# Performance work log

Hardware: AMD Instinct MI355X
Metric: run time of the kernel (lower is better)

## Reference

```python
import jax, jax.numpy as jnp
import numpy as np

D_MODEL = 1024
D_FFN = 4096
H = 16
D_HEAD = D_MODEL // H
B, L = 2, 2048
EPS = 1e-6


def layer_norm(x, a, b):
    # Matches torch: std is unbiased (ddof=1), and divides by (std + eps)
    mean = jnp.mean(x, axis=-1, keepdims=True)
    var = jnp.sum((x - mean) ** 2, axis=-1, keepdims=True) / (x.shape[-1] - 1)
    std = jnp.sqrt(var)
    return (x - mean) / (std + EPS) * a + b


def setup_inputs() -> dict:
    key = jax.random.key(0)
    ks = jax.random.split(key, 10)
    s = 0.02
    x = jax.random.normal(ks[0], (B, L, D_MODEL), dtype=jnp.float32)
    mask = jnp.tril(jnp.ones((L, L), dtype=jnp.int32))[None, None]  # causal [1,1,L,L]
    return {
        "x": x,
        "mask": mask,
        "Wqkv": jax.random.normal(ks[1], (D_MODEL, 3 * D_MODEL), jnp.float32) * s,
        "bqkv": jnp.zeros((3 * D_MODEL,), jnp.float32),
        "Wo": jax.random.normal(ks[2], (D_MODEL, D_MODEL), jnp.float32) * s,
        "bo": jnp.zeros((D_MODEL,), jnp.float32),
        "W1": jax.random.normal(ks[3], (D_MODEL, D_FFN), jnp.float32) * s,
        "b1": jnp.zeros((D_FFN,), jnp.float32),
        "W2": jax.random.normal(ks[4], (D_FFN, D_MODEL), jnp.float32) * s,
        "b2": jnp.zeros((D_MODEL,), jnp.float32),
        "ln1_a": jnp.ones((D_MODEL,), jnp.float32),
        "ln1_b": jnp.zeros((D_MODEL,), jnp.float32),
        "ln2_a": jnp.ones((D_MODEL,), jnp.float32),
        "ln2_b": jnp.zeros((D_MODEL,), jnp.float32),
    }


def reference(x, mask, Wqkv, bqkv, Wo, bo, W1, b1, W2, b2, ln1_a, ln1_b, ln2_a, ln2_b):
    b, l, d = x.shape
    # --- attention sublayer ---
    qkv = x @ Wqkv + bqkv                                   # [b, l, 3*d]
    qkv = qkv.reshape(b, l, 3, H, D_HEAD)                   # '(three h d)' ordering
    q, k, v = qkv[:, :, 0], qkv[:, :, 1], qkv[:, :, 2]      # each [b, l, h, dh]
    scores = jnp.einsum('bqhd,bkhd->bhqk', q, k) / jnp.sqrt(
        jnp.asarray(D_HEAD, x.dtype))                        # [b, h, lq, lk]
    scores = jnp.where(mask == 0, -jnp.inf, scores)
    p = jax.nn.softmax(scores, axis=-1)
    attn = jnp.einsum('bhqk,bkhd->bqhd', p, v).reshape(b, l, d)
    attn_out = attn @ Wo + bo
    x = layer_norm(x + attn_out, ln1_a, ln1_b)
    # --- MLP sublayer ---
    h = jax.nn.relu(x @ W1 + b1)
    mlp_out = h @ W2 + b2
    return layer_norm(x + mlp_out, ln2_a, ln2_b)
```

## Files before the change

kernel.cpp:

```cpp
#include <hip/hip_runtime.h>

#define D_MODEL 1024
#define D_FFN   4096
#define NH      16
#define DH      64
#define BB      2
#define LL      2048
#define MROWS   (BB * LL)

typedef unsigned short u16;
typedef unsigned int   u32;
typedef short bf16x8 __attribute__((ext_vector_type(8)));
typedef float f32x4  __attribute__((ext_vector_type(4)));

__device__ __forceinline__ float bf2f(u16 u) {
    union { u32 i; float f; } v;
    v.i = ((u32)u) << 16;
    return v.f;
}
__device__ __forceinline__ u16 f2bf(float f) {
    union { float f; u32 i; } v;
    v.f = f;
    u32 x = v.i;
    x += 0x7fffu + ((x >> 16) & 1u);
    return (u16)(x >> 16);
}
__device__ __forceinline__ u32 pack_bf_trunc(float a, float b) {
    return __builtin_amdgcn_perm(__float_as_uint(b), __float_as_uint(a),
                                 0x07060302u);
}

typedef const __attribute__((address_space(1))) u32 gu32;
typedef __attribute__((address_space(3))) u32 lu32;
__device__ __forceinline__ void gload_lds16(const void* g, void* l) {
    __builtin_amdgcn_global_load_lds((gu32*)g, (lu32*)l, 16, 0, 0);
}

__global__ __launch_bounds__(256) void prep_kernel(
    const float* __restrict__ x,    u16* __restrict__ xb,
    const float* __restrict__ Wqkv, u16* __restrict__ Wqkvt,
    const float* __restrict__ Wo,   u16* __restrict__ Wot,
    const float* __restrict__ W1,   u16* __restrict__ W1t,
    const float* __restrict__ W2,   u16* __restrict__ W2t)
{
    __shared__ float tile[64][65];
    const int tid = threadIdx.x;
    const int bi  = blockIdx.x;

    if (bi < 2048) {
        int i = bi * 2048 + tid * 8;
        float4 a = *(const float4*)(x + i);
        float4 b = *(const float4*)(x + i + 4);
        u16 o[8] = {f2bf(a.x), f2bf(a.y), f2bf(a.z), f2bf(a.w),
                    f2bf(b.x), f2bf(b.y), f2bf(b.z), f2bf(b.w)};
        *(uint4*)(xb + i) = *(const uint4*)o;
        return;
    }

    const float* W; u16* Wt; int K, N, t;
    if (bi < 2816)      { W = Wqkv; Wt = Wqkvt; K = 1024; N = 3072; t = bi - 2048; }
    else if (bi < 3072) { W = Wo;   Wt = Wot;   K = 1024; N = 1024; t = bi - 2816; }
    else if (bi < 4096) { W = W1;   Wt = W1t;   K = 1024; N = 4096; t = bi - 3072; }
    else                { W = W2;   Wt = W2t;   K = 4096; N = 1024; t = bi - 4096; }
    const int ntiles = N >> 6;
    const int n0 = (t % ntiles) * 64;
    const int k0 = (t / ntiles) * 64;

    int kr = tid >> 4;
    int nc = (tid & 15) * 4;
    #pragma unroll
    for (int p = 0; p < 4; ++p) {
        float4 v = *(const float4*)&W[(size_t)(k0 + kr + p * 16) * N + n0 + nc];
        tile[kr + p * 16][nc + 0] = v.x;
        tile[kr + p * 16][nc + 1] = v.y;
        tile[kr + p * 16][nc + 2] = v.z;
        tile[kr + p * 16][nc + 3] = v.w;
    }
    __syncthreads();

    int nr = tid >> 2;
    int kc = (tid & 3) * 16;
    u16 o[16];
    #pragma unroll
    for (int j = 0; j < 16; ++j) o[j] = f2bf(tile[kc + j][nr]);
    u16* dst = &Wt[(size_t)(n0 + nr) * K + k0 + kc];
    *(uint4*)dst       = *(const uint4*)&o[0];
    *(uint4*)(dst + 8) = *(const uint4*)&o[8];
}

template <int EPI, int RF32, int OF32, int KS>
__global__ __launch_bounds__(256) void gemm_bt_kernel(
    const u16* __restrict__ A, const u16* __restrict__ Bt,
    const float* __restrict__ bias, const void* __restrict__ resv,
    void* __restrict__ out0v, u16* __restrict__ out1, u16* __restrict__ out2,
    int M, int N, int K)
{
    __shared__ u16 sA[128 * 64];
    __shared__ u16 sB[128 * 64];

    const int tid  = threadIdx.x;
    const int lane = tid & 63;
    const int wave = tid >> 6;
    const int wm   = (wave & 1) * 64;
    const int wn   = (wave >> 1) * 64;
    const int quad = lane >> 4;
    const int l16  = lane & 15;

    const int nb  = gridDim.x;
    const int mb  = gridDim.y;
    const int f   = blockIdx.y * nb + blockIdx.x;
    const int xcd = f & 7;
    const int idx = f >> 3;
    const int rn  = nb >> 1;
    const int rm  = mb >> 2;
    const int n0  = ((xcd & 1) * rn + (idx % rn)) * 128;
    const int ym  = (xcd >> 1) * rm + (idx / rn);

    int s, m0;
    if (KS > 1) {
        const int mt = mb / KS;
        s  = ym / mt;
        m0 = (ym % mt) * 128;
    } else {
        s  = 0;
        m0 = ym * 128;
    }
    const int Kseg = K / KS;
    const int kbeg = s * Kseg;

    f32x4 acc[4][4];
    #pragma unroll
    for (int i = 0; i < 4; ++i)
        #pragma unroll
        for (int j = 0; j < 4; ++j)
            acc[i][j] = (f32x4){0.f, 0.f, 0.f, 0.f};

    const u16* Ablk = A  + (size_t)m0 * K;
    const u16* Bblk = Bt + (size_t)n0 * K;

    for (int k0 = kbeg; k0 < kbeg + Kseg; k0 += 64) {
        #pragma unroll
        for (int i = 0; i < 4; ++i) {
            int chunk = (i * 4 + wave) * 64 + lane;
            int r = chunk >> 3;
            int c = (chunk & 7) ^ (r & 7);
            size_t goff = (size_t)r * K + k0 + c * 8;
            gload_lds16(Ablk + goff, &sA[(i * 4 + wave) * 512]);
            gload_lds16(Bblk + goff, &sB[(i * 4 + wave) * 512]);
        }
        __syncthreads();

        #pragma unroll
        for (int ks = 0; ks < 2; ++ks) {
            bf16x8 af[4], bfr[4];
            #pragma unroll
            for (int i = 0; i < 4; ++i) {
                int R = wm + i * 16 + l16;
                int slot = R * 8 + ((ks * 4 + quad) ^ (R & 7));
                af[i] = *(const bf16x8*)&sA[slot * 8];
            }
            #pragma unroll
            for (int j = 0; j < 4; ++j) {
                int R = wn + j * 16 + l16;
                int slot = R * 8 + ((ks * 4 + quad) ^ (R & 7));
                bfr[j] = *(const bf16x8*)&sB[slot * 8];
            }
            #pragma unroll
            for (int i = 0; i < 4; ++i)
                #pragma unroll
                for (int j = 0; j < 4; ++j)
                    acc[i][j] = __builtin_amdgcn_mfma_f32_16x16x32_bf16(
                        af[i], bfr[j], acc[i][j], 0, 0, 0);
        }
        __syncthreads();
    }

    #pragma unroll
    for (int i = 0; i < 4; ++i) {
        int rowb = m0 + wm + i * 16 + quad * 4;
        #pragma unroll
        for (int j = 0; j < 4; ++j) {
            int col = n0 + wn + j * 16 + l16;
            float bv = (EPI == 3) ? 0.f : bias[col];
            #pragma unroll
            for (int r = 0; r < 4; ++r) {
                int rr = rowb + r;
                float v = acc[i][j][r] + bv;
                if (EPI == 0) {
                    int which = col >> 10;
                    int h     = (col >> 6) & 15;
                    int d     = col & 63;
                    int b     = rr >> 11;
                    int l     = rr & 2047;
                    size_t idx2 = ((size_t)(b * NH + h) * LL + l) * DH + d;
                    u16* o0 = (u16*)out0v;
                    if (which == 0)      o0[idx2]   = f2bf(v * 0.125f);
                    else if (which == 1) out1[idx2] = f2bf(v);
                    else                 out2[idx2] = f2bf(v);
                } else if (EPI == 3) {
                    ((u16*)out0v)[((size_t)s * M + rr) * N + col] = f2bf(v);
                } else {
                    size_t idx2 = (size_t)rr * N + col;
                    if (EPI == 1) {
                        v += RF32 ? ((const float*)resv)[idx2]
                                  : bf2f(((const u16*)resv)[idx2]);
                    } else {
                        v = v > 0.f ? v : 0.f;
                    }
                    if (OF32) ((float*)out0v)[idx2] = v;
                    else      ((u16*)out0v)[idx2]   = f2bf(v);
                }
            }
        }
    }
}

template <int KS, int RF32, int OF32>
__global__ __launch_bounds__(256) void lnfuse_kernel(
    const u16* __restrict__ P, const float* __restrict__ bias,
    const void* __restrict__ resv,
    const float* __restrict__ ga, const float* __restrict__ gb,
    void* __restrict__ outv)
{
    __shared__ float red[8];
    const int tid  = threadIdx.x;
    const int lane = tid & 63;
    const int wave = tid >> 6;
    const size_t row = blockIdx.x;
    const size_t SL  = (size_t)MROWS * D_MODEL;
    const int c = tid * 4;

    float v0, v1, v2, v3;
    {
        float4 bv = *(const float4*)(bias + c);
        v0 = bv.x; v1 = bv.y; v2 = bv.z; v3 = bv.w;
    }
    #pragma unroll
    for (int s = 0; s < KS; ++s) {
        uint2 p = *(const uint2*)(P + s * SL + row * D_MODEL + c);
        v0 += bf2f((u16)p.x); v1 += bf2f((u16)(p.x >> 16));
        v2 += bf2f((u16)p.y); v3 += bf2f((u16)(p.y >> 16));
    }
    if (RF32) {
        float4 r = *(const float4*)((const float*)resv + row * D_MODEL + c);
        v0 += r.x; v1 += r.y; v2 += r.z; v3 += r.w;
    } else {
        uint2 r = *(const uint2*)((const u16*)resv + row * D_MODEL + c);
        v0 += bf2f((u16)r.x); v1 += bf2f((u16)(r.x >> 16));
        v2 += bf2f((u16)r.y); v3 += bf2f((u16)(r.y >> 16));
    }

    float s_ = v0 + v1 + v2 + v3;
    #pragma unroll
    for (int o = 32; o > 0; o >>= 1) s_ += __shfl_xor(s_, o, 64);
    if (lane == 0) red[wave] = s_;
    __syncthreads();
    float mean = (red[0] + red[1] + red[2] + red[3]) * (1.f / 1024.f);

    float d0 = v0 - mean, d1 = v1 - mean, d2 = v2 - mean, d3 = v3 - mean;
    float q = d0 * d0 + d1 * d1 + d2 * d2 + d3 * d3;
    #pragma unroll
    for (int o = 32; o > 0; o >>= 1) q += __shfl_xor(q, o, 64);
    if (lane == 0) red[4 + wave] = q;
    __syncthreads();
    float var = (red[4] + red[5] + red[6] + red[7]) * (1.f / 1023.f);
    float inv = 1.f / (sqrtf(var) + 1e-6f);

    float y0 = d0 * inv * ga[c + 0] + gb[c + 0];
    float y1 = d1 * inv * ga[c + 1] + gb[c + 1];
    float y2 = d2 * inv * ga[c + 2] + gb[c + 2];
    float y3 = d3 * inv * ga[c + 3] + gb[c + 3];
    if (OF32) {
        float4 y = {y0, y1, y2, y3};
        *(float4*)((float*)outv + row * D_MODEL + c) = y;
    } else {
        ushort4 y = {f2bf(y0), f2bf(y1), f2bf(y2), f2bf(y3)};
        *(ushort4*)((u16*)outv + row * D_MODEL + c) = y;
    }
}

__global__ __launch_bounds__(256) void attn_kernel(
    const u16* __restrict__ Q, const u16* __restrict__ K,
    const u16* __restrict__ V, u16* __restrict__ out)
{
    __shared__ u16 ks[64 * 72];
    __shared__ u16 vs[64 * 72];
    __shared__ u16 ps[4][2][16 * 72];

    const int tid  = threadIdx.x;
    const int lane = tid & 63;
    const int wave = tid >> 6;
    const int l16  = lane & 15;
    const int quad = lane >> 4;

    const int f   = blockIdx.x;
    const int xcd = f & 7;
    const int idx = f >> 3;
    const int bh  = xcd * 4 + (idx >> 4);
    const int pr  = idx & 15;
    const int b   = bh >> 4, h = bh & 15;
    const size_t head_off = (size_t)bh * LL * DH;

    const u16* Qh = Q + head_off;
    const u16* Kh = K + head_off;
    const u16* Vh = V + head_off;

    const int qtA = 31 - pr, qtB = pr;
    const int baseA = qtA * 64 + wave * 16;
    const int baseB = qtB * 64 + wave * 16;
    const int qgA   = baseA + l16;
    const int qgB   = baseB + l16;

    const bf16x8 qfA0 = *(const bf16x8*)&Qh[(size_t)qgA * DH + quad * 8];
    const bf16x8 qfA1 = *(const bf16x8*)&Qh[(size_t)qgA * DH + 32 + quad * 8];
    const bf16x8 qfB0 = *(const bf16x8*)&Qh[(size_t)qgB * DH + quad * 8];
    const bf16x8 qfB1 = *(const bf16x8*)&Qh[(size_t)qgB * DH + 32 + quad * 8];

    float lA = 0.f, lB = 0.f;
    f32x4 oA[4], oB[4];
    #pragma unroll
    for (int t = 0; t < 4; ++t) {
        oA[t] = (f32x4){0.f, 0.f, 0.f, 0.f};
        oB[t] = (f32x4){0.f, 0.f, 0.f, 0.f};
    }

    u16* psA = &ps[wave][0][0];
    u16* psB = &ps[wave][1][0];

    const int key = tid >> 2;
    const int kd0 = (tid & 3) * 16;
    const int kp  = tid >> 3;
    const int vd0 = (tid & 7) * 8;

    uint4 kr0, kr1, vr0, vr1;
    {
        const u16* ksrc = Kh + (size_t)key * DH + kd0;
        kr0 = *(const uint4*)ksrc;
        kr1 = *(const uint4*)(ksrc + 8);
        const u16* vsrc = Vh + (size_t)(2 * kp) * DH + vd0;
        vr0 = *(const uint4*)vsrc;
        vr1 = *(const uint4*)(vsrc + DH);
    }

    for (int c = 0; c <= qtA; ++c) {
        const bool doB = (c <= qtB);
        __syncthreads();
        *(uint4*)&ks[key * 72 + kd0]     = kr0;
        *(uint4*)&ks[key * 72 + kd0 + 8] = kr1;
        {
            const u32* w0 = (const u32*)&vr0;
            const u32* w1 = (const u32*)&vr1;
            #pragma unroll
            for (int e = 0; e < 8; ++e) {
                int d = vd0 + e;
                u32 lo = (w0[e >> 1] >> ((e & 1) * 16)) & 0xffffu;
                u32 hi = (w1[e >> 1] >> ((e & 1) * 16)) & 0xffffu;
                int csw = kp ^ (4 * ((d >> 3) & 7));
                *(u32*)&vs[d * 72 + 2 * csw] = lo | (hi << 16);
            }
        }
        __syncthreads();
        if (c < qtA) {
            const u16* ksrc = Kh + (size_t)((c + 1) * 64 + key) * DH + kd0;
            kr0 = *(const uint4*)ksrc;
            kr1 = *(const uint4*)(ksrc + 8);
            const u16* vsrc = Vh + (size_t)((c + 1) * 64 + 2 * kp) * DH + vd0;
            vr0 = *(const uint4*)vsrc;
            vr1 = *(const uint4*)(vsrc + DH);
        }

        f32x4 stA[4], stB[4];
        #pragma unroll
        for (int t = 0; t < 4; ++t) {
            bf16x8 k0 = *(const bf16x8*)&ks[(t * 16 + l16) * 72 + quad * 8];
            bf16x8 k1 = *(const bf16x8*)&ks[(t * 16 + l16) * 72 + 32 + quad * 8];
            f32x4 s = (f32x4){0.f, 0.f, 0.f, 0.f};
            s = __builtin_amdgcn_mfma_f32_16x16x32_bf16(k0, qfA0, s, 0, 0, 0);
            s = __builtin_amdgcn_mfma_f32_16x16x32_bf16(k1, qfA1, s, 0, 0, 0);
            stA[t] = s;
            if (doB) {
                f32x4 s2 = (f32x4){0.f, 0.f, 0.f, 0.f};
                s2 = __builtin_amdgcn_mfma_f32_16x16x32_bf16(k0, qfB0, s2, 0, 0, 0);
                s2 = __builtin_amdgcn_mfma_f32_16x16x32_bf16(k1, qfB1, s2, 0, 0, 0);
                stB[t] = s2;
            }
        }

        if (c == qtA) {
            #pragma unroll
            for (int t = 0; t < 4; ++t)
                #pragma unroll
                for (int r = 0; r < 4; ++r)
                    if (c * 64 + t * 16 + quad * 4 + r > qgA) stA[t][r] = -INFINITY;
        }
        if (doB && c == qtB) {
            #pragma unroll
            for (int t = 0; t < 4; ++t)
                #pragma unroll
                for (int r = 0; r < 4; ++r)
                    if (c * 64 + t * 16 + quad * 4 + r > qgB) stB[t][r] = -INFINITY;
        }

        {
            float psum = 0.f;
            #pragma unroll
            for (int t = 0; t < 4; ++t) {
                float p0 = __expf(stA[t][0]), p1 = __expf(stA[t][1]);
                float p2 = __expf(stA[t][2]), p3 = __expf(stA[t][3]);
                psum += (p0 + p1) + (p2 + p3);
                uint2 w = {pack_bf_trunc(p0, p1), pack_bf_trunc(p2, p3)};
                *(uint2*)&psA[l16 * 72 + t * 16 + quad * 4] = w;
            }
            psum += __shfl_xor(psum, 16, 64);
            psum += __shfl_xor(psum, 32, 64);
            lA += psum;
        }
        if (doB) {
            float psum = 0.f;
            #pragma unroll
            for (int t = 0; t < 4; ++t) {
                float p0 = __expf(stB[t][0]), p1 = __expf(stB[t][1]);
                float p2 = __expf(stB[t][2]), p3 = __expf(stB[t][3]);
                psum += (p0 + p1) + (p2 + p3);
                uint2 w = {pack_bf_trunc(p0, p1), pack_bf_trunc(p2, p3)};
                *(uint2*)&psB[l16 * 72 + t * 16 + quad * 4] = w;
            }
            psum += __shfl_xor(psum, 16, 64);
            psum += __shfl_xor(psum, 32, 64);
            lB += psum;
        }

        bf16x8 pfA0 = *(const bf16x8*)&psA[l16 * 72 + quad * 8];
        bf16x8 pfA1 = *(const bf16x8*)&psA[l16 * 72 + 32 + quad * 8];
        bf16x8 pfB0, pfB1;
        if (doB) {
            pfB0 = *(const bf16x8*)&psB[l16 * 72 + quad * 8];
            pfB1 = *(const bf16x8*)&psB[l16 * 72 + 32 + quad * 8];
        }

        #pragma unroll
        for (int dt = 0; dt < 4; ++dt) {
            int d  = dt * 16 + l16;
            int sw = 4 * ((d >> 3) & 7);
            bf16x8 vf0 = *(const bf16x8*)&vs[d * 72 + 2 * ((quad * 4) ^ sw)];
            bf16x8 vf1 = *(const bf16x8*)&vs[d * 72 + 2 * ((16 + quad * 4) ^ sw)];
            oA[dt] = __builtin_amdgcn_mfma_f32_16x16x32_bf16(pfA0, vf0, oA[dt], 0, 0, 0);
            oA[dt] = __builtin_amdgcn_mfma_f32_16x16x32_bf16(pfA1, vf1, oA[dt], 0, 0, 0);
            if (doB) {
                oB[dt] = __builtin_amdgcn_mfma_f32_16x16x32_bf16(pfB0, vf0, oB[dt], 0, 0, 0);
                oB[dt] = __builtin_amdgcn_mfma_f32_16x16x32_bf16(pfB1, vf1, oB[dt], 0, 0, 0);
            }
        }
    }

    {
        float i0 = 1.f / __shfl(lA, quad * 4 + 0, 64);
        float i1 = 1.f / __shfl(lA, quad * 4 + 1, 64);
        float i2 = 1.f / __shfl(lA, quad * 4 + 2, 64);
        float i3 = 1.f / __shfl(lA, quad * 4 + 3, 64);
        #pragma unroll
        for (int dt = 0; dt < 4; ++dt) {
            size_t col = h * DH + dt * 16 + l16;
            size_t r0  = ((size_t)b * LL + baseA + quad * 4) * D_MODEL + col;
            out[r0]               = f2bf(oA[dt][0] * i0);
            out[r0 + D_MODEL]     = f2bf(oA[dt][1] * i1);
            out[r0 + 2 * D_MODEL] = f2bf(oA[dt][2] * i2);
            out[r0 + 3 * D_MODEL] = f2bf(oA[dt][3] * i3);
        }
    }
    {
        float i0 = 1.f / __shfl(lB, quad * 4 + 0, 64);
        float i1 = 1.f / __shfl(lB, quad * 4 + 1, 64);
        float i2 = 1.f / __shfl(lB, quad * 4 + 2, 64);
        float i3 = 1.f / __shfl(lB, quad * 4 + 3, 64);
        #pragma unroll
        for (int dt = 0; dt < 4; ++dt) {
            size_t col = h * DH + dt * 16 + l16;
            size_t r0  = ((size_t)b * LL + baseB + quad * 4) * D_MODEL + col;
            out[r0]               = f2bf(oB[dt][0] * i0);
            out[r0 + D_MODEL]     = f2bf(oB[dt][1] * i1);
            out[r0 + 2 * D_MODEL] = f2bf(oB[dt][2] * i2);
            out[r0 + 3 * D_MODEL] = f2bf(oB[dt][3] * i3);
        }
    }
}

extern "C" void kernel_launch(void* const* d_in, const int* in_sizes, int n_in,
                              void* d_out, int out_size, void* d_ws, size_t ws_size,
                              hipStream_t stream)
{
    const float* x    = (const float*)d_in[0];
    const float* Wqkv = (const float*)d_in[2];
    const float* bqkv = (const float*)d_in[3];
    const float* Wo   = (const float*)d_in[4];
    const float* bo   = (const float*)d_in[5];
    const float* W1   = (const float*)d_in[6];
    const float* b1   = (const float*)d_in[7];
    const float* W2   = (const float*)d_in[8];
    const float* b2   = (const float*)d_in[9];
    const float* ln1a = (const float*)d_in[10];
    const float* ln1b = (const float*)d_in[11];
    const float* ln2a = (const float*)d_in[12];
    const float* ln2b = (const float*)d_in[13];

    char* ws = (char*)d_ws;
    const size_t HSZ = (size_t)BB * NH * LL * DH;
    u16*   Qp    = (u16*)ws;
    u16*   Kp    = Qp + HSZ;
    u16*   Vp    = Kp + HSZ;
    u16*   attn  = Vp + HSZ;
    u16*   hbuf  = (u16*)ws;
    u16*   xb    = (u16*)(ws + 33554432);
    u16*   x1    = (u16*)(ws + 50331648);
    u16*   Wqkvt = (u16*)(ws + 58720256);
    u16*   Wot   = (u16*)(ws + 65011712);
    u16*   W1t   = (u16*)(ws + 67108864);
    u16*   W2t   = (u16*)(ws + 75497472);
    u16*   Pbuf  = (u16*)(ws + 83886080);

    dim3 blk(256);

    prep_kernel<<<dim3(5120), blk, 0, stream>>>(
        x, xb, Wqkv, Wqkvt, Wo, Wot, W1, W1t, W2, W2t);

    gemm_bt_kernel<0,0,0,1><<<dim3(24, 32), blk, 0, stream>>>(
        xb, Wqkvt, bqkv, nullptr, Qp, Kp, Vp, MROWS, 3 * D_MODEL, D_MODEL);
    attn_kernel<<<dim3(512), blk, 0, stream>>>(Qp, Kp, Vp, attn);
    gemm_bt_kernel<3,0,0,2><<<dim3(8, 64), blk, 0, stream>>>(
        attn, Wot, bo, nullptr, Pbuf, nullptr, nullptr, MROWS, D_MODEL, D_MODEL);
    lnfuse_kernel<2,1,0><<<dim3(MROWS), blk, 0, stream>>>(
        Pbuf, bo, x, ln1a, ln1b, x1);
    gemm_bt_kernel<2,0,0,1><<<dim3(32, 32), blk, 0, stream>>>(
        x1, W1t, b1, nullptr, hbuf, nullptr, nullptr, MROWS, D_FFN, D_MODEL);
    gemm_bt_kernel<3,0,0,4><<<dim3(8, 128), blk, 0, stream>>>(
        hbuf, W2t, b2, nullptr, Pbuf, nullptr, nullptr, MROWS, D_MODEL, D_FFN);
    lnfuse_kernel<4,0,1><<<dim3(MROWS), blk, 0, stream>>>(
        Pbuf, b2, x1, ln2a, ln2b, d_out);
}
```

Baseline: 346.4 us.

## Split attention KV range in two halves and merge partial outputs

Each attention block now handles only half of the key range for its paired query tiles, so the grid doubles to 1024 blocks. Unnormalized partial outputs and row sums go to workspace, and a new merge kernel adds the two halves, normalizes them and writes the final attention layout. The goal is more blocks in flight to fill the GPU better. In exchange it adds an extra kernel launch and a round trip of the partial outputs through global memory. It also drops the register prefetch of the next K/V tile, so global loads are no longer overlapped with compute.

New measurement: 361.7 us. +4.4%, slower.

```diff
diff --git a/kernel.cpp b/kernel.cpp
--- a/kernel.cpp
+++ b/kernel.cpp
@@ -281,7 +281,7 @@
 
 __global__ __launch_bounds__(256) void attn_kernel(
     const u16* __restrict__ Q, const u16* __restrict__ K,
-    const u16* __restrict__ V, u16* __restrict__ out)
+    const u16* __restrict__ V, u16* __restrict__ Ob, float* __restrict__ lb)
 {
     __shared__ u16 ks[64 * 72];
     __shared__ u16 vs[64 * 72];
@@ -293,12 +293,13 @@
     const int l16  = lane & 15;
     const int quad = lane >> 4;
 
-    const int f   = blockIdx.x;
-    const int xcd = f & 7;
-    const int idx = f >> 3;
-    const int bh  = xcd * 4 + (idx >> 4);
-    const int pr  = idx & 15;
-    const int b   = bh >> 4, h = bh & 15;
+    const int f    = blockIdx.x;
+    const int xcd  = f & 7;
+    const int idx  = f >> 3;
+    const int bh   = xcd * 4 + (idx >> 5);
+    const int rem  = idx & 31;
+    const int pr   = rem >> 1;
+    const int half = rem & 1;
     const size_t head_off = (size_t)bh * LL * DH;
 
     const u16* Qh = Q + head_off;
@@ -306,6 +307,17 @@
     const u16* Vh = V + head_off;
 
     const int qtA = 31 - pr, qtB = pr;
+    const int hA = (qtA + 2) >> 1;
+    const int hB = (qtB + 2) >> 1;
+    int aS, aE, bS, bE;
+    if (!half) { aS = 0;  aE = hA;      bS = 0;  bE = hB; }
+    else       { aS = hA; aE = qtA + 1; bS = hB; bE = qtB + 1; }
+    int  sgS[3], sgE[3];
+    bool sgA[3], sgB[3];
+    sgS[0] = bS;               sgE[0] = min(bE, aS); sgA[0] = false; sgB[0] = true;
+    sgS[1] = aS;               sgE[1] = min(aE, bE); sgA[1] = true;  sgB[1] = true;
+    sgS[2] = max(aS, bE);      sgE[2] = aE;          sgA[2] = true;  sgB[2] = false;
+
     const int baseA = qtA * 64 + wave * 16;
     const int baseB = qtB * 64 + wave * 16;
     const int qgA   = baseA + l16;
@@ -332,157 +344,169 @@
     const int kp  = tid >> 3;
     const int vd0 = (tid & 7) * 8;
 
-    uint4 kr0, kr1, vr0, vr1;
-    {
-        const u16* ksrc = Kh + (size_t)key * DH + kd0;
-        kr0 = *(const uint4*)ksrc;
-        kr1 = *(const uint4*)(ksrc + 8);
-        const u16* vsrc = Vh + (size_t)(2 * kp) * DH + vd0;
-        vr0 = *(const uint4*)vsrc;
-        vr1 = *(const uint4*)(vsrc + DH);
-    }
-
-    for (int c = 0; c <= qtA; ++c) {
-        const bool doB = (c <= qtB);
-        __syncthreads();
-        *(uint4*)&ks[key * 72 + kd0]     = kr0;
-        *(uint4*)&ks[key * 72 + kd0 + 8] = kr1;
-        {
-            const u32* w0 = (const u32*)&vr0;
-            const u32* w1 = (const u32*)&vr1;
-            #pragma unroll
-            for (int e = 0; e < 8; ++e) {
-                int d = vd0 + e;
-                u32 lo = (w0[e >> 1] >> ((e & 1) * 16)) & 0xffffu;
-                u32 hi = (w1[e >> 1] >> ((e & 1) * 16)) & 0xffffu;
-                int csw = kp ^ (4 * ((d >> 3) & 7));
-                *(u32*)&vs[d * 72 + 2 * csw] = lo | (hi << 16);
-            }
-        }
-        __syncthreads();
-        if (c < qtA) {
-            const u16* ksrc = Kh + (size_t)((c + 1) * 64 + key) * DH + kd0;
-            kr0 = *(const uint4*)ksrc;
-            kr1 = *(const uint4*)(ksrc + 8);
-            const u16* vsrc = Vh + (size_t)((c + 1) * 64 + 2 * kp) * DH + vd0;
-            vr0 = *(const uint4*)vsrc;
-            vr1 = *(const uint4*)(vsrc + DH);
-        }
-
-        f32x4 stA[4], stB[4];
-        #pragma unroll
-        for (int t = 0; t < 4; ++t) {
-            bf16x8 k0 = *(const bf16x8*)&ks[(t * 16 + l16) * 72 + quad * 8];
-            bf16x8 k1 = *(const bf16x8*)&ks[(t * 16 + l16) * 72 + 32 + quad * 8];
-            f32x4 s = (f32x4){0.f, 0.f, 0.f, 0.f};
-            s = __builtin_amdgcn_mfma_f32_16x16x32_bf16(k0, qfA0, s, 0, 0, 0);
-            s = __builtin_amdgcn_mfma_f32_16x16x32_bf16(k1, qfA1, s, 0, 0, 0);
-            stA[t] = s;
-            if (doB) {
-                f32x4 s2 = (f32x4){0.f, 0.f, 0.f, 0.f};
-                s2 = __builtin_amdgcn_mfma_f32_16x16x32_bf16(k0, qfB0, s2, 0, 0, 0);
-                s2 = __builtin_amdgcn_mfma_f32_16x16x32_bf16(k1, qfB1, s2, 0, 0, 0);
-                stB[t] = s2;
-            }
-        }
-
-        if (c == qtA) {
-            #pragma unroll
-            for (int t = 0; t < 4; ++t)
+    for (int sg = 0; sg < 3; ++sg) {
+        const bool dA = sgA[sg], dB = sgB[sg];
+        for (int c = sgS[sg]; c < sgE[sg]; ++c) {
+            __syncthreads();
+            {
+                const u16* src = Kh + (size_t)(c * 64 + key) * DH + kd0;
+                *(uint4*)&ks[key * 72 + kd0]     = *(const uint4*)src;
+                *(uint4*)&ks[key * 72 + kd0 + 8] = *(const uint4*)(src + 8);
+            }
+            {
+                const u16* src = Vh + (size_t)(c * 64 + 2 * kp) * DH + vd0;
+                uint4 v0 = *(const uint4*)src;
+                uint4 v1 = *(const uint4*)(src + DH);
+                const u32* w0 = (const u32*)&v0;
+                const u32* w1 = (const u32*)&v1;
                 #pragma unroll
-                for (int r = 0; r < 4; ++r)
-                    if (c * 64 + t * 16 + quad * 4 + r > qgA) stA[t][r] = -INFINITY;
-        }
-        if (doB && c == qtB) {
-            #pragma unroll
-            for (int t = 0; t < 4; ++t)
-                #pragma unroll
-                for (int r = 0; r < 4; ++r)
-                    if (c * 64 + t * 16 + quad * 4 + r > qgB) stB[t][r] = -INFINITY;
-        }
-
-        {
-            float psum = 0.f;
+                for (int e = 0; e < 8; ++e) {
+                    int d = vd0 + e;
+                    u32 lo = (w0[e >> 1] >> ((e & 1) * 16)) & 0xffffu;
+                    u32 hi = (w1[e >> 1] >> ((e & 1) * 16)) & 0xffffu;
+                    int csw = kp ^ (4 * ((d >> 3) & 7));
+                    *(u32*)&vs[d * 72 + 2 * csw] = lo | (hi << 16);
+                }
+            }
+            __syncthreads();
+
+            f32x4 stA[4], stB[4];
             #pragma unroll
             for (int t = 0; t < 4; ++t) {
-                float p0 = __expf(stA[t][0]), p1 = __expf(stA[t][1]);
-                float p2 = __expf(stA[t][2]), p3 = __expf(stA[t][3]);
-                psum += (p0 + p1) + (p2 + p3);
-                uint2 w = {pack_bf_trunc(p0, p1), pack_bf_trunc(p2, p3)};
-                *(uint2*)&psA[l16 * 72 + t * 16 + quad * 4] = w;
-            }
-            psum += __shfl_xor(psum, 16, 64);
-            psum += __shfl_xor(psum, 32, 64);
-            lA += psum;
+                bf16x8 k0 = *(const bf16x8*)&ks[(t * 16 + l16) * 72 + quad * 8];
+                bf16x8 k1 = *(const bf16x8*)&ks[(t * 16 + l16) * 72 + 32 + quad * 8];
+                if (dA) {
+                    f32x4 s = (f32x4){0.f, 0.f, 0.f, 0.f};
+                    s = __builtin_amdgcn_mfma_f32_16x16x32_bf16(k0, qfA0, s, 0, 0, 0);
+                    s = __builtin_amdgcn_mfma_f32_16x16x32_bf16(k1, qfA1, s, 0, 0, 0);
+                    stA[t] = s;
+                }
+                if (dB) {
+                    f32x4 s2 = (f32x4){0.f, 0.f, 0.f, 0.f};
+                    s2 = __builtin_amdgcn_mfma_f32_16x16x32_bf16(k0, qfB0, s2, 0, 0, 0);
+                    s2 = __builtin_amdgcn_mfma_f32_16x16x32_bf16(k1, qfB1, s2, 0, 0, 0);
+                    stB[t] = s2;
+                }
+            }
+
+            if (dA && c == qtA) {
+                #pragma unroll
+                for (int t = 0; t < 4; ++t)
+                    #pragma unroll
+                    for (int r = 0; r < 4; ++r)
+                        if (c * 64 + t * 16 + quad * 4 + r > qgA) stA[t][r] = -INFINITY;
+            }
+            if (dB && c == qtB) {
+                #pragma unroll
+                for (int t = 0; t < 4; ++t)
+                    #pragma unroll
+                    for (int r = 0; r < 4; ++r)
+                        if (c * 64 + t * 16 + quad * 4 + r > qgB) stB[t][r] = -INFINITY;
+            }
+
+            if (dA) {
+                float psum = 0.f;
+                #pragma unroll
+                for (int t = 0; t < 4; ++t) {
+                    float p0 = __expf(stA[t][0]), p1 = __expf(stA[t][1]);
+                    float p2 = __expf(stA[t][2]), p3 = __expf(stA[t][3]);
+                    psum += (p0 + p1) + (p2 + p3);
+                    uint2 w = {pack_bf_trunc(p0, p1), pack_bf_trunc(p2, p3)};
+                    *(uint2*)&psA[l16 * 72 + t * 16 + quad * 4] = w;
+                }
+                psum += __shfl_xor(psum, 16, 64);
+                psum += __shfl_xor(psum, 32, 64);
+                lA += psum;
+            }
+            if (dB) {
+                float psum = 0.f;
+                #pragma unroll
+                for (int t = 0; t < 4; ++t) {
+                    float p0 = __expf(stB[t][0]), p1 = __expf(stB[t][1]);
+                    float p2 = __expf(stB[t][2]), p3 = __expf(stB[t][3]);
+                    psum += (p0 + p1) + (p2 + p3);
+                    uint2 w = {pack_bf_trunc(p0, p1), pack_bf_trunc(p2, p3)};
+                    *(uint2*)&psB[l16 * 72 + t * 16 + quad * 4] = w;
+                }
+                psum += __shfl_xor(psum, 16, 64);
+                psum += __shfl_xor(psum, 32, 64);
+                lB += psum;
+            }
+
+            bf16x8 pfA0, pfA1, pfB0, pfB1;
+            if (dA) {
+                pfA0 = *(const bf16x8*)&psA[l16 * 72 + quad * 8];
+                pfA1 = *(const bf16x8*)&psA[l16 * 72 + 32 + quad * 8];
+            }
+            if (dB) {
+                pfB0 = *(const bf16x8*)&psB[l16 * 72 + quad * 8];
+                pfB1 = *(const bf16x8*)&psB[l16 * 72 + 32 + quad * 8];
+            }
+
+            #pragma unroll
+            for (int dt = 0; dt < 4; ++dt) {
+                int d  = dt * 16 + l16;
+                int sw = 4 * ((d >> 3) & 7);
+                bf16x8 vf0 = *(const bf16x8*)&vs[d * 72 + 2 * ((quad * 4) ^ sw)];
+                bf16x8 vf1 = *(const bf16x8*)&vs[d * 72 + 2 * ((16 + quad * 4) ^ sw)];
+                if (dA) {
+                    oA[dt] = __builtin_amdgcn_mfma_f32_16x16x32_bf16(pfA0, vf0, oA[dt], 0, 0, 0);
+                    oA[dt] = __builtin_amdgcn_mfma_f32_16x16x32_bf16(pfA1, vf1, oA[dt], 0, 0, 0);
+                }
+                if (dB) {
+                    oB[dt] = __builtin_amdgcn_mfma_f32_16x16x32_bf16(pfB0, vf0, oB[dt], 0, 0, 0);
+                    oB[dt] = __builtin_amdgcn_mfma_f32_16x16x32_bf16(pfB1, vf1, oB[dt], 0, 0, 0);
+                }
+            }
         }
-        if (doB) {
-            float psum = 0.f;
-            #pragma unroll
-            for (int t = 0; t < 4; ++t) {
-                float p0 = __expf(stB[t][0]), p1 = __expf(stB[t][1]);
-                float p2 = __expf(stB[t][2]), p3 = __expf(stB[t][3]);
-                psum += (p0 + p1) + (p2 + p3);
-                uint2 w = {pack_bf_trunc(p0, p1), pack_bf_trunc(p2, p3)};
-                *(uint2*)&psB[l16 * 72 + t * 16 + quad * 4] = w;
-            }
-            psum += __shfl_xor(psum, 16, 64);
-            psum += __shfl_xor(psum, 32, 64);
-            lB += psum;
-        }
-
-        bf16x8 pfA0 = *(const bf16x8*)&psA[l16 * 72 + quad * 8];
-        bf16x8 pfA1 = *(const bf16x8*)&psA[l16 * 72 + 32 + quad * 8];
-        bf16x8 pfB0, pfB1;
-        if (doB) {
-            pfB0 = *(const bf16x8*)&psB[l16 * 72 + quad * 8];
-            pfB1 = *(const bf16x8*)&psB[l16 * 72 + 32 + quad * 8];
-        }
-
-        #pragma unroll
-        for (int dt = 0; dt < 4; ++dt) {
-            int d  = dt * 16 + l16;
-            int sw = 4 * ((d >> 3) & 7);
-            bf16x8 vf0 = *(const bf16x8*)&vs[d * 72 + 2 * ((quad * 4) ^ sw)];
-            bf16x8 vf1 = *(const bf16x8*)&vs[d * 72 + 2 * ((16 + quad * 4) ^ sw)];
-            oA[dt] = __builtin_amdgcn_mfma_f32_16x16x32_bf16(pfA0, vf0, oA[dt], 0, 0, 0);
-            oA[dt] = __builtin_amdgcn_mfma_f32_16x16x32_bf16(pfA1, vf1, oA[dt], 0, 0, 0);
-            if (doB) {
-                oB[dt] = __builtin_amdgcn_mfma_f32_16x16x32_bf16(pfB0, vf0, oB[dt], 0, 0, 0);
-                oB[dt] = __builtin_amdgcn_mfma_f32_16x16x32_bf16(pfB1, vf1, oB[dt], 0, 0, 0);
-            }
-        }
-    }
-
-    {
-        float i0 = 1.f / __shfl(lA, quad * 4 + 0, 64);
-        float i1 = 1.f / __shfl(lA, quad * 4 + 1, 64);
-        float i2 = 1.f / __shfl(lA, quad * 4 + 2, 64);
-        float i3 = 1.f / __shfl(lA, quad * 4 + 3, 64);
-        #pragma unroll
-        for (int dt = 0; dt < 4; ++dt) {
-            size_t col = h * DH + dt * 16 + l16;
-            size_t r0  = ((size_t)b * LL + baseA + quad * 4) * D_MODEL + col;
-            out[r0]               = f2bf(oA[dt][0] * i0);
-            out[r0 + D_MODEL]     = f2bf(oA[dt][1] * i1);
-            out[r0 + 2 * D_MODEL] = f2bf(oA[dt][2] * i2);
-            out[r0 + 3 * D_MODEL] = f2bf(oA[dt][3] * i3);
-        }
-    }
-    {
-        float i0 = 1.f / __shfl(lB, quad * 4 + 0, 64);
-        float i1 = 1.f / __shfl(lB, quad * 4 + 1, 64);
-        float i2 = 1.f / __shfl(lB, quad * 4 + 2, 64);
-        float i3 = 1.f / __shfl(lB, quad * 4 + 3, 64);
-        #pragma unroll
-        for (int dt = 0; dt < 4; ++dt) {
-            size_t col = h * DH + dt * 16 + l16;
-            size_t r0  = ((size_t)b * LL + baseB + quad * 4) * D_MODEL + col;
-            out[r0]               = f2bf(oB[dt][0] * i0);
-            out[r0 + D_MODEL]     = f2bf(oB[dt][1] * i1);
-            out[r0 + 2 * D_MODEL] = f2bf(oB[dt][2] * i2);
-            out[r0 + 3 * D_MODEL] = f2bf(oB[dt][3] * i3);
-        }
-    }
+    }
+
+    const size_t hb = (size_t)(half * 32 + bh) * LL;
+    #pragma unroll
+    for (int dt = 0; dt < 4; ++dt) {
+        size_t r0 = (hb + baseA + quad * 4) * 64 + dt * 16 + l16;
+        Ob[r0]        = f2bf(oA[dt][0]);
+        Ob[r0 + 64]   = f2bf(oA[dt][1]);
+        Ob[r0 + 128]  = f2bf(oA[dt][2]);
+        Ob[r0 + 192]  = f2bf(oA[dt][3]);
+        size_t r1 = (hb + baseB + quad * 4) * 64 + dt * 16 + l16;
+        Ob[r1]        = f2bf(oB[dt][0]);
+        Ob[r1 + 64]   = f2bf(oB[dt][1]);
+        Ob[r1 + 128]  = f2bf(oB[dt][2]);
+        Ob[r1 + 192]  = f2bf(oB[dt][3]);
+    }
+    if (quad == 0) {
+        lb[hb + qgA] = lA;
+        lb[hb + qgB] = lB;
+    }
+}
+
+__global__ __launch_bounds__(256) void attn_merge_kernel(
+    const u16* __restrict__ Ob, const float* __restrict__ lb,
+    u16* __restrict__ out)
+{
+    const int i   = blockIdx.x * 256 + threadIdx.x;
+    const int row = i >> 3;
+    const int d0  = (i & 7) * 8;
+    const int bh  = row >> 11, rowl = row & 2047;
+    const int b   = bh >> 4, h = bh & 15;
+    const size_t HOFF = (size_t)32 * LL * 64;
+
+    uint4 p0 = *(const uint4*)&Ob[(size_t)row * 64 + d0];
+    uint4 p1 = *(const uint4*)&Ob[HOFF + (size_t)row * 64 + d0];
+    float inv = 1.f / (lb[row] + lb[32 * LL + row]);
+
+    const u32* w0 = (const u32*)&p0;
+    const u32* w1 = (const u32*)&p1;
+    u16 o[8];
+    #pragma unroll
+    for (int e = 0; e < 8; ++e) {
+        float v = bf2f((u16)(w0[e >> 1] >> ((e & 1) * 16)))
+                + bf2f((u16)(w1[e >> 1] >> ((e & 1) * 16)));
+        o[e] = f2bf(v * inv);
+    }
+    *(uint4*)&out[((size_t)b * LL + rowl) * D_MODEL + h * DH + d0] =
+        *(const uint4*)o;
 }
 
 extern "C" void kernel_launch(void* const* d_in, const int* in_sizes, int n_in,
@@ -511,8 +535,10 @@
     u16*   attn  = Vp + HSZ;
     u16*   hbuf  = (u16*)ws;
     u16*   xb    = (u16*)(ws + 33554432);
+    u16*   Obuf  = (u16*)(ws + 33554432);
     u16*   x1    = (u16*)(ws + 50331648);
     u16*   Wqkvt = (u16*)(ws + 58720256);
+    float* lbuf  = (float*)(ws + 58720256);
     u16*   Wot   = (u16*)(ws + 65011712);
     u16*   W1t   = (u16*)(ws + 67108864);
     u16*   W2t   = (u16*)(ws + 75497472);
@@ -525,7 +551,8 @@
 
     gemm_bt_kernel<0,0,0,1><<<dim3(24, 32), blk, 0, stream>>>(
         xb, Wqkvt, bqkv, nullptr, Qp, Kp, Vp, MROWS, 3 * D_MODEL, D_MODEL);
-    attn_kernel<<<dim3(512), blk, 0, stream>>>(Qp, Kp, Vp, attn);
+    attn_kernel<<<dim3(1024), blk, 0, stream>>>(Qp, Kp, Vp, Obuf, lbuf);
+    attn_merge_kernel<<<dim3(2048), blk, 0, stream>>>(Obuf, lbuf, attn);
     gemm_bt_kernel<3,0,0,2><<<dim3(8, 64), blk, 0, stream>>>(
         attn, Wot, bo, nullptr, Pbuf, nullptr, nullptr, MROWS, D_MODEL, D_MODEL);
     lnfuse_kernel<2,1,0><<<dim3(MROWS), blk, 0, stream>>>(
```

## Move Wo/W1/W2 weight conversion into attention kernel as extra blocks

Applied to the files above, without the earlier changes.

Weight transposes and bf16 conversions for Wo, W1 and W2 move out of the prep kernel and into extra blocks appended to the attention launch. Prep now converts only x and Wqkv, which shortens the work ahead of the QKV GEMM. The memory-bound weight conversion can then overlap with the compute-bound, causally imbalanced attention blocks. Attention shared memory becomes one flat buffer reused as the transpose tile, which adds complexity and could affect how attention blocks are scheduled.

Result: faster. 333.6 us (-3.7%).

```diff
diff --git a/kernel.cpp b/kernel.cpp
--- a/kernel.cpp
+++ b/kernel.cpp
@@ -36,14 +36,41 @@
     __builtin_amdgcn_global_load_lds((gu32*)g, (lu32*)l, 16, 0, 0);
 }
 
+__device__ __forceinline__ void wt_tile(
+    const float* __restrict__ W, u16* __restrict__ Wt,
+    int K, int N, int t, int tid, float* tile )
+{
+    const int ntiles = N >> 6;
+    const int n0 = (t % ntiles) * 64;
+    const int k0 = (t / ntiles) * 64;
+
+    int kr = tid >> 4;
+    int nc = (tid & 15) * 4;
+    #pragma unroll
+    for (int p = 0; p < 4; ++p) {
+        float4 v = *(const float4*)&W[(size_t)(k0 + kr + p * 16) * N + n0 + nc];
+        tile[(kr + p * 16) * 65 + nc + 0] = v.x;
+        tile[(kr + p * 16) * 65 + nc + 1] = v.y;
+        tile[(kr + p * 16) * 65 + nc + 2] = v.z;
+        tile[(kr + p * 16) * 65 + nc + 3] = v.w;
+    }
+    __syncthreads();
+
+    int nr = tid >> 2;
+    int kc = (tid & 3) * 16;
+    u16 o[16];
+    #pragma unroll
+    for (int j = 0; j < 16; ++j) o[j] = f2bf(tile[(kc + j) * 65 + nr]);
+    u16* dst = &Wt[(size_t)(n0 + nr) * K + k0 + kc];
+    *(uint4*)dst       = *(const uint4*)&o[0];
+    *(uint4*)(dst + 8) = *(const uint4*)&o[8];
+}
+
 __global__ __launch_bounds__(256) void prep_kernel(
     const float* __restrict__ x,    u16* __restrict__ xb,
-    const float* __restrict__ Wqkv, u16* __restrict__ Wqkvt,
-    const float* __restrict__ Wo,   u16* __restrict__ Wot,
-    const float* __restrict__ W1,   u16* __restrict__ W1t,
-    const float* __restrict__ W2,   u16* __restrict__ W2t)
+    const float* __restrict__ Wqkv, u16* __restrict__ Wqkvt)
 {
-    __shared__ float tile[64][65];
+    __shared__ float tile[64 * 65];
     const int tid = threadIdx.x;
     const int bi  = blockIdx.x;
 
@@ -56,36 +83,7 @@
         *(uint4*)(xb + i) = *(const uint4*)o;
         return;
     }
-
-    const float* W; u16* Wt; int K, N, t;
-    if (bi < 2816)      { W = Wqkv; Wt = Wqkvt; K = 1024; N = 3072; t = bi - 2048; }
-    else if (bi < 3072) { W = Wo;   Wt = Wot;   K = 1024; N = 1024; t = bi - 2816; }
-    else if (bi < 4096) { W = W1;   Wt = W1t;   K = 1024; N = 4096; t = bi - 3072; }
-    else                { W = W2;   Wt = W2t;   K = 4096; N = 1024; t = bi - 4096; }
-    const int ntiles = N >> 6;
-    const int n0 = (t % ntiles) * 64;
-    const int k0 = (t / ntiles) * 64;
-
-    int kr = tid >> 4;
-    int nc = (tid & 15) * 4;
-    #pragma unroll
-    for (int p = 0; p < 4; ++p) {
-        float4 v = *(const float4*)&W[(size_t)(k0 + kr + p * 16) * N + n0 + nc];
-        tile[kr + p * 16][nc + 0] = v.x;
-        tile[kr + p * 16][nc + 1] = v.y;
-        tile[kr + p * 16][nc + 2] = v.z;
-        tile[kr + p * 16][nc + 3] = v.w;
-    }
-    __syncthreads();
-
-    int nr = tid >> 2;
-    int kc = (tid & 3) * 16;
-    u16 o[16];
-    #pragma unroll
-    for (int j = 0; j < 16; ++j) o[j] = f2bf(tile[kc + j][nr]);
-    u16* dst = &Wt[(size_t)(n0 + nr) * K + k0 + kc];
-    *(uint4*)dst       = *(const uint4*)&o[0];
-    *(uint4*)(dst + 8) = *(const uint4*)&o[8];
+    wt_tile(Wqkv, Wqkvt, 1024, 3072, bi - 2048, tid, tile);
 }
 
 template <int EPI, int RF32, int OF32, int KS>
@@ -281,19 +279,34 @@
 
 __global__ __launch_bounds__(256) void attn_kernel(
     const u16* __restrict__ Q, const u16* __restrict__ K,
-    const u16* __restrict__ V, u16* __restrict__ out)
+    const u16* __restrict__ V, u16* __restrict__ out,
+    const float* __restrict__ Wo, u16* __restrict__ Wot,
+    const float* __restrict__ W1, u16* __restrict__ W1t,
+    const float* __restrict__ W2, u16* __restrict__ W2t)
 {
-    __shared__ u16 ks[64 * 72];
-    __shared__ u16 vs[64 * 72];
-    __shared__ u16 ps[4][2][16 * 72];
+    __shared__ u16 smem[18432];
+    u16* ks = smem;
+    u16* vs = smem + 4608;
+    u16* ps = smem + 9216;
 
     const int tid  = threadIdx.x;
+    const int bi   = blockIdx.x;
+
+    if (bi >= 512) {
+        float* tile = (float*)smem;
+        int t = bi - 512;
+        if (t < 256)       wt_tile(Wo, Wot, 1024, 1024, t,        tid, tile);
+        else if (t < 1280) wt_tile(W1, W1t, 1024, 4096, t - 256,  tid, tile);
+        else               wt_tile(W2, W2t, 4096, 1024, t - 1280, tid, tile);
+        return;
+    }
+
     const int lane = tid & 63;
     const int wave = tid >> 6;
     const int l16  = lane & 15;
     const int quad = lane >> 4;
 
-    const int f   = blockIdx.x;
+    const int f   = bi;
     const int xcd = f & 7;
     const int idx = f >> 3;
     const int bh  = xcd * 4 + (idx >> 4);
@@ -324,8 +337,8 @@
         oB[t] = (f32x4){0.f, 0.f, 0.f, 0.f};
     }
 
-    u16* psA = &ps[wave][0][0];
-    u16* psB = &ps[wave][1][0];
+    u16* psA = ps + wave * 2304;
+    u16* psB = psA + 1152;
 
     const int key = tid >> 2;
     const int kd0 = (tid & 3) * 16;
@@ -520,12 +533,12 @@
 
     dim3 blk(256);
 
-    prep_kernel<<<dim3(5120), blk, 0, stream>>>(
-        x, xb, Wqkv, Wqkvt, Wo, Wot, W1, W1t, W2, W2t);
+    prep_kernel<<<dim3(2816), blk, 0, stream>>>(x, xb, Wqkv, Wqkvt);
 
     gemm_bt_kernel<0,0,0,1><<<dim3(24, 32), blk, 0, stream>>>(
         xb, Wqkvt, bqkv, nullptr, Qp, Kp, Vp, MROWS, 3 * D_MODEL, D_MODEL);
-    attn_kernel<<<dim3(512), blk, 0, stream>>>(Qp, Kp, Vp, attn);
+    attn_kernel<<<dim3(2816), blk, 0, stream>>>(
+        Qp, Kp, Vp, attn, Wo, Wot, W1, W1t, W2, W2t);
     gemm_bt_kernel<3,0,0,2><<<dim3(8, 64), blk, 0, stream>>>(
         attn, Wot, bo, nullptr, Pbuf, nullptr, nullptr, MROWS, D_MODEL, D_MODEL);
     lnfuse_kernel<2,1,0><<<dim3(MROWS), blk, 0, stream>>>(
```
